# Kernel tuning notes

Hardware: AMD Instinct MI355X
Metric: run time of the kernel (lower is better)

## Reference

```python
import jax, jax.numpy as jnp
import numpy as np

ROW_DIMS = (8, 10, 20, 20)   # factorization of vocab = 32000
COL_DIMS = (4, 4, 6, 8)      # factorization of out_features = 768
RANKS = (1, 16, 16, 16, 1)
VOCAB = int(np.prod(ROW_DIMS))
OUT = int(np.prod(COL_DIMS))
# cum_prod[k] = prod(ROW_DIMS[k+1:]) -> mixed-radix digit extraction
CUM_PROD = np.concatenate([np.cumprod(ROW_DIMS[::-1])[::-1][1:], [1]]).astype(np.int32)


def setup_inputs() -> dict:
    key = jax.random.key(0)
    ks = jax.random.split(key, 5)
    x = jax.random.randint(ks[0], (8, 4096), 0, VOCAB, dtype=jnp.int32)
    cores = {}
    for k in range(4):
        shp = (RANKS[k], ROW_DIMS[k], COL_DIMS[k], RANKS[k + 1])
        # scale so that the product of 4 cores has ~unit stddev per element
        std = 1.0 / np.sqrt(RANKS[k + 1])
        cores[f"core{k}"] = (jax.random.normal(ks[k + 1], shp, dtype=jnp.float32) * std)
    return {"x": x, **cores}


def reference(x, core0, core1, core2, core3):
    cores = (core0, core1, core2, core3)
    idx = x.reshape(-1)                 # [B] flattened token indices
    B = idx.shape[0]
    digits = [(idx // CUM_PROD[k]) % ROW_DIMS[k] for k in range(4)]
    # first core: [1, n0, m0, r1] -> gather -> [B, m0, r1]
    res = core0[0][digits[0]].reshape(B, COL_DIMS[0], RANKS[1])
    for k in range(1, 4):
        g = jnp.take(cores[k], digits[k], axis=1)        # [r_k, B, m_k, r_{k+1}]
        res = jnp.einsum('bar,rbms->bams', res, g)       # chain contraction over rank
        res = res.reshape(B, -1, RANKS[k + 1])
    rows = res.reshape(B, OUT)
    return rows.reshape(*x.shape, OUT)
```

## Files before the change

kernel.cpp:

```cpp
#include <hip/hip_runtime.h>


#define NTOK 32768
#define TPW  8
#define NBLK (NTOK / (4 * TPW))
#define G2A01_BYTES (400 * 64 * 16)
#define G2A2_BYTES  (400 * 64 * 8)
#define G1B_BYTES   (80 * 64 * 8)
#define TBL_BYTES   (G2A01_BYTES + G2A2_BYTES + G1B_BYTES)

typedef _Float16 f16x4 __attribute__((ext_vector_type(4)));
typedef _Float16 f16x8 __attribute__((ext_vector_type(8)));
typedef float f32x4 __attribute__((ext_vector_type(4)));

__device__ inline unsigned pack2(float x, float y) {
    _Float16 hx = (_Float16)x, hy = (_Float16)y;
    unsigned short ux = __builtin_bit_cast(unsigned short, hx);
    unsigned short uy = __builtin_bit_cast(unsigned short, hy);
    return (unsigned)ux | ((unsigned)uy << 16);
}

__global__ __launch_bounds__(256) void build_frag_tables(const float* __restrict__ core0,
                                                         const float* __restrict__ core1,
                                                         const float* __restrict__ core2,
                                                         const float* __restrict__ core3,
                                                         unsigned* __restrict__ g2a01,
                                                         unsigned* __restrict__ g2a2,
                                                         unsigned* __restrict__ g1b) {
    __shared__ float lds[768];
    int b = blockIdx.x, t = threadIdx.x;
    int l = t & 63, part = t >> 6;
    if (b < 400) {
        int d2 = b / 20, d3 = b % 20;
#pragma unroll
        for (int i = 0; i < 3; ++i) {
            int f = t + i * 256;
            int r2 = f / 48, mc = f - r2 * 48;
            int m2 = mc >> 3, m3 = mc & 7;
            float acc = 0.f;
#pragma unroll
            for (int r3 = 0; r3 < 16; ++r3)
                acc += core2[((r2 * 20 + d2) * 6 + m2) * 16 + r3] *
                       core3[(r3 * 20 + d3) * 8 + m3];
            lds[f] = acc;
        }
        __syncthreads();
        {
            int pp = part >> 1;
            int jp = part & 1;
            int k = ((l >> 4) << 2) + jp * 2;
            int mc = pp * 16 + (l & 15);
            g2a01[(b * 64 + l) * 4 + part] = pack2(lds[k * 48 + mc],
                                                   lds[(k + 1) * 48 + mc]);
        }
        if (part < 2) {
            int k = ((l >> 4) << 2) + part * 2;
            int mc = 32 + (l & 15);
            g2a2[(b * 64 + l) * 2 + part] = pack2(lds[k * 48 + mc],
                                                  lds[(k + 1) * 48 + mc]);
        }
    } else {
        int combo = b - 400;
        int d0 = combo / 10, d1 = combo % 10;
        int a = t >> 4, r2 = t & 15;
        int a0 = a >> 2, m1 = a & 3;
        float acc = 0.f;
#pragma unroll
        for (int r1 = 0; r1 < 16; ++r1)
            acc += core0[(d0 * 4 + a0) * 16 + r1] *
                   core1[((r1 * 10 + d1) * 4 + m1) * 16 + r2];
        lds[t] = acc;
        __syncthreads();
        if (part < 2) {
            int k = ((l >> 4) << 2) + part * 2;
            int n = l & 15;
            g1b[(combo * 64 + l) * 2 + part] = pack2(lds[n * 16 + k],
                                                     lds[n * 16 + k + 1]);
        }
    }
}

struct Frag { f16x8 a01; f16x4 a2; f16x4 b; };

__device__ inline Frag load_frag(int id, int lane,
                                 const f16x8* __restrict__ g2a01,
                                 const f16x4* __restrict__ g2a2,
                                 const f16x4* __restrict__ g1b) {
    Frag f;
    int c23 = id % 400, c01 = id / 400;
    f.a01 = g2a01[c23 * 64 + lane];
    f.a2  = g2a2[c23 * 64 + lane];
    f.b   = g1b[c01 * 64 + lane];
    return f;
}

__global__ __launch_bounds__(256) void te_mfma(const int* __restrict__ x,
                                               const f16x8* __restrict__ g2a01,
                                               const f16x4* __restrict__ g2a2,
                                               const f16x4* __restrict__ g1b,
                                               float* __restrict__ out) {
    const int wave = threadIdx.x >> 6, lane = threadIdx.x & 63;
    const int tok0 = (blockIdx.x * 4 + wave) * TPW;

    int4 xa = ((const int4*)(x + tok0))[0];
    int4 xb = ((const int4*)(x + tok0))[1];
    int idxs[TPW] = {xa.x, xa.y, xa.z, xa.w, xb.x, xb.y, xb.z, xb.w};

    Frag f0 = load_frag(idxs[0], lane, g2a01, g2a2, g1b);
    Frag f1 = load_frag(idxs[1], lane, g2a01, g2a2, g1b);

    const f32x4 z = {0.f, 0.f, 0.f, 0.f};
    float* obase = out + (size_t)tok0 * 768 + (lane & 15) * 48 + ((lane >> 4) << 2);

#pragma unroll
    for (int t = 0; t < TPW; ++t) {
        Frag f2 = f1;
        if (t + 2 < TPW)
            f2 = load_frag(idxs[t + 2], lane, g2a01, g2a2, g1b);

        f16x4 a0 = __builtin_shufflevector(f0.a01, f0.a01, 0, 1, 2, 3);
        f16x4 a1 = __builtin_shufflevector(f0.a01, f0.a01, 4, 5, 6, 7);
        f32x4 d0 = __builtin_amdgcn_mfma_f32_16x16x16f16(a0,    f0.b, z, 0, 0, 0);
        f32x4 d1 = __builtin_amdgcn_mfma_f32_16x16x16f16(a1,    f0.b, z, 0, 0, 0);
        f32x4 d2 = __builtin_amdgcn_mfma_f32_16x16x16f16(f0.a2, f0.b, z, 0, 0, 0);

        float* o = obase + t * 768;
        *(f32x4*)(o)      = d0;
        *(f32x4*)(o + 16) = d1;
        *(f32x4*)(o + 32) = d2;

        f0 = f1; f1 = f2;
    }
}

__global__ void te_direct(const int* __restrict__ x,
                          const float* __restrict__ core0,
                          const float* __restrict__ core1,
                          const float* __restrict__ core2,
                          const float* __restrict__ core3,
                          float* __restrict__ out) {
    int tok = blockIdx.x;
    int lane = threadIdx.x;
    int idx = x[tok];
    int d0 = idx / 4000;
    int rem = idx - d0 * 4000;
    int d1 = rem / 400;
    rem -= d1 * 400;
    int d2 = rem / 20;
    int d3 = rem - d2 * 20;
    float* o = out + (size_t)tok * 768;
    for (int p = 0; p < 3; ++p) {
        int base = (p * 64 + lane) * 4;
        int a = base / 48;
        int mc = base - a * 48;
        int a0 = a >> 2, m1 = a & 3;
        float s[16];
#pragma unroll
        for (int r2 = 0; r2 < 16; ++r2) {
            float acc = 0.f;
            for (int r1 = 0; r1 < 16; ++r1)
                acc += core0[(d0 * 4 + a0) * 16 + r1] *
                       core1[((r1 * 10 + d1) * 4 + m1) * 16 + r2];
            s[r2] = acc;
        }
        float4 accv = {0.f, 0.f, 0.f, 0.f};
        float* accp = (float*)&accv;
        for (int j = 0; j < 4; ++j) {
            int mcj = mc + j;
            int m2 = mcj >> 3, m3 = mcj & 7;
            float tt = 0.f;
            for (int r2 = 0; r2 < 16; ++r2) {
                float g = 0.f;
                for (int r3 = 0; r3 < 16; ++r3)
                    g += core2[((r2 * 20 + d2) * 6 + m2) * 16 + r3] *
                         core3[(r3 * 20 + d3) * 8 + m3];
                tt += s[r2] * g;
            }
            accp[j] = tt;
        }
        *(float4*)(o + base) = accv;
    }
}

extern "C" void kernel_launch(void* const* d_in, const int* in_sizes, int n_in,
                              void* d_out, int out_size, void* d_ws, size_t ws_size,
                              hipStream_t stream) {
    const int*   x     = (const int*)d_in[0];
    const float* core0 = (const float*)d_in[1];
    const float* core1 = (const float*)d_in[2];
    const float* core2 = (const float*)d_in[3];
    const float* core3 = (const float*)d_in[4];
    float* out = (float*)d_out;

    if (ws_size >= (size_t)TBL_BYTES) {
        unsigned* g2a01 = (unsigned*)d_ws;
        unsigned* g2a2  = (unsigned*)((char*)d_ws + G2A01_BYTES);
        unsigned* g1b   = (unsigned*)((char*)d_ws + G2A01_BYTES + G2A2_BYTES);
        build_frag_tables<<<480, 256, 0, stream>>>(core0, core1, core2, core3,
                                                   g2a01, g2a2, g1b);
        te_mfma<<<NBLK, 256, 0, stream>>>(x, (const f16x8*)g2a01,
                                          (const f16x4*)g2a2,
                                          (const f16x4*)g1b, out);
    } else {
        te_direct<<<NTOK, 64, 0, stream>>>(x, core0, core1, core2, core3, out);
    }
}
```

Before: 27.66 us.

## Interleave core2/3 fragment tables into padded records, split builder blocks, double tokens per wave

Merges the two core2/core3 fragment tables into one 32-byte-per-lane record, so each token's A fragments come from one contiguous region instead of two tables. The table builder now splits each (d2,d3) combo across two blocks (880 blocks instead of 480) to spread the precompute over more CUs. The main kernel processes 16 tokens per wave instead of 8, halving the grid to 512 blocks. The padded record wastes 8 bytes per lane, and the smaller grid may leave some CUs underused.

```diff
diff --git a/kernel.cpp b/kernel.cpp
--- a/kernel.cpp
+++ b/kernel.cpp
@@ -2,12 +2,11 @@
 
 
 #define NTOK 32768
-#define TPW  8
+#define TPW  16
 #define NBLK (NTOK / (4 * TPW))
-#define G2A01_BYTES (400 * 64 * 16)
-#define G2A2_BYTES  (400 * 64 * 8)
+#define G2REC_BYTES (400 * 64 * 32)
 #define G1B_BYTES   (80 * 64 * 8)
-#define TBL_BYTES   (G2A01_BYTES + G2A2_BYTES + G1B_BYTES)
+#define TBL_BYTES   (G2REC_BYTES + G1B_BYTES)
 
 typedef _Float16 f16x4 __attribute__((ext_vector_type(4)));
 typedef _Float16 f16x8 __attribute__((ext_vector_type(8)));
@@ -24,43 +23,44 @@
                                                          const float* __restrict__ core1,
                                                          const float* __restrict__ core2,
                                                          const float* __restrict__ core3,
-                                                         unsigned* __restrict__ g2a01,
-                                                         unsigned* __restrict__ g2a2,
+                                                         unsigned* __restrict__ g2rec,
                                                          unsigned* __restrict__ g1b) {
     __shared__ float lds[768];
     int b = blockIdx.x, t = threadIdx.x;
     int l = t & 63, part = t >> 6;
-    if (b < 400) {
-        int d2 = b / 20, d3 = b % 20;
-#pragma unroll
-        for (int i = 0; i < 3; ++i) {
-            int f = t + i * 256;
-            int r2 = f / 48, mc = f - r2 * 48;
+    if (b < 800) {
+        int c23 = b >> 1, half = b & 1;
+        int d2 = c23 / 20, d3 = c23 % 20;
+        int niter = half ? 1 : 2;
+#pragma unroll
+        for (int i = 0; i < 2; ++i) {
+            if (i >= niter) break;
+            int v = t + i * 256;
+            int mcw = half ? 16 : 32;
+            int r2 = v / mcw;
+            int mc = (half ? 32 : 0) + (v - r2 * mcw);
             int m2 = mc >> 3, m3 = mc & 7;
             float acc = 0.f;
 #pragma unroll
             for (int r3 = 0; r3 < 16; ++r3)
                 acc += core2[((r2 * 20 + d2) * 6 + m2) * 16 + r3] *
                        core3[(r3 * 20 + d3) * 8 + m3];
-            lds[f] = acc;
+            lds[r2 * 48 + mc] = acc;
         }
         __syncthreads();
-        {
-            int pp = part >> 1;
-            int jp = part & 1;
+        unsigned* rec = g2rec + (size_t)c23 * 512 + l * 8;
+        if (half == 0) {
+            int pp = part >> 1, jp = part & 1;
             int k = ((l >> 4) << 2) + jp * 2;
             int mc = pp * 16 + (l & 15);
-            g2a01[(b * 64 + l) * 4 + part] = pack2(lds[k * 48 + mc],
-                                                   lds[(k + 1) * 48 + mc]);
-        }
-        if (part < 2) {
+            rec[part] = pack2(lds[k * 48 + mc], lds[(k + 1) * 48 + mc]);
+        } else if (part < 2) {
             int k = ((l >> 4) << 2) + part * 2;
             int mc = 32 + (l & 15);
-            g2a2[(b * 64 + l) * 2 + part] = pack2(lds[k * 48 + mc],
-                                                  lds[(k + 1) * 48 + mc]);
+            rec[4 + part] = pack2(lds[k * 48 + mc], lds[(k + 1) * 48 + mc]);
         }
     } else {
-        int combo = b - 400;
+        int combo = b - 800;
         int d0 = combo / 10, d1 = combo % 10;
         int a = t >> 4, r2 = t & 15;
         int a0 = a >> 2, m1 = a & 3;
@@ -83,31 +83,34 @@
 struct Frag { f16x8 a01; f16x4 a2; f16x4 b; };
 
 __device__ inline Frag load_frag(int id, int lane,
-                                 const f16x8* __restrict__ g2a01,
-                                 const f16x4* __restrict__ g2a2,
+                                 const unsigned* __restrict__ g2rec,
                                  const f16x4* __restrict__ g1b) {
     Frag f;
     int c23 = id % 400, c01 = id / 400;
-    f.a01 = g2a01[c23 * 64 + lane];
-    f.a2  = g2a2[c23 * 64 + lane];
+    const unsigned* rec = g2rec + (size_t)c23 * 512 + lane * 8;
+    f.a01 = *(const f16x8*)rec;
+    f.a2  = *(const f16x4*)(rec + 4);
     f.b   = g1b[c01 * 64 + lane];
     return f;
 }
 
 __global__ __launch_bounds__(256) void te_mfma(const int* __restrict__ x,
-                                               const f16x8* __restrict__ g2a01,
-                                               const f16x4* __restrict__ g2a2,
+                                               const unsigned* __restrict__ g2rec,
                                                const f16x4* __restrict__ g1b,
                                                float* __restrict__ out) {
     const int wave = threadIdx.x >> 6, lane = threadIdx.x & 63;
     const int tok0 = (blockIdx.x * 4 + wave) * TPW;
 
-    int4 xa = ((const int4*)(x + tok0))[0];
-    int4 xb = ((const int4*)(x + tok0))[1];
-    int idxs[TPW] = {xa.x, xa.y, xa.z, xa.w, xb.x, xb.y, xb.z, xb.w};
-
-    Frag f0 = load_frag(idxs[0], lane, g2a01, g2a2, g1b);
-    Frag f1 = load_frag(idxs[1], lane, g2a01, g2a2, g1b);
+    int idxs[TPW];
+#pragma unroll
+    for (int i = 0; i < TPW / 4; ++i) {
+        int4 xv = ((const int4*)(x + tok0))[i];
+        idxs[i * 4 + 0] = xv.x; idxs[i * 4 + 1] = xv.y;
+        idxs[i * 4 + 2] = xv.z; idxs[i * 4 + 3] = xv.w;
+    }
+
+    Frag f0 = load_frag(idxs[0], lane, g2rec, g1b);
+    Frag f1 = load_frag(idxs[1], lane, g2rec, g1b);
 
     const f32x4 z = {0.f, 0.f, 0.f, 0.f};
     float* obase = out + (size_t)tok0 * 768 + (lane & 15) * 48 + ((lane >> 4) << 2);
@@ -116,7 +119,7 @@
     for (int t = 0; t < TPW; ++t) {
         Frag f2 = f1;
         if (t + 2 < TPW)
-            f2 = load_frag(idxs[t + 2], lane, g2a01, g2a2, g1b);
+            f2 = load_frag(idxs[t + 2], lane, g2rec, g1b);
 
         f16x4 a0 = __builtin_shufflevector(f0.a01, f0.a01, 0, 1, 2, 3);
         f16x4 a1 = __builtin_shufflevector(f0.a01, f0.a01, 4, 5, 6, 7);
@@ -193,14 +196,11 @@
     float* out = (float*)d_out;
 
     if (ws_size >= (size_t)TBL_BYTES) {
-        unsigned* g2a01 = (unsigned*)d_ws;
-        unsigned* g2a2  = (unsigned*)((char*)d_ws + G2A01_BYTES);
-        unsigned* g1b   = (unsigned*)((char*)d_ws + G2A01_BYTES + G2A2_BYTES);
-        build_frag_tables<<<480, 256, 0, stream>>>(core0, core1, core2, core3,
-                                                   g2a01, g2a2, g1b);
-        te_mfma<<<NBLK, 256, 0, stream>>>(x, (const f16x8*)g2a01,
-                                          (const f16x4*)g2a2,
-                                          (const f16x4*)g1b, out);
+        unsigned* g2rec = (unsigned*)d_ws;
+        unsigned* g1b   = (unsigned*)((char*)d_ws + G2REC_BYTES);
+        build_frag_tables<<<880, 256, 0, stream>>>(core0, core1, core2, core3,
+                                                   g2rec, g1b);
+        te_mfma<<<NBLK, 256, 0, stream>>>(x, g2rec, (const f16x4*)g1b, out);
     } else {
         te_direct<<<NTOK, 64, 0, stream>>>(x, core0, core1, core2, core3, out);
     }
```

Measured after the change: 28.27 us. +2.2%, slower.
